# Kernel optimization log

Measured on AMD Instinct MI355X. Metric: run time of the kernel, lower is better.

Reference implementation:

```python
import jax, jax.numpy as jnp
import numpy as np

EPS = 1e-5

def setup_inputs() -> dict:
    key = jax.random.key(0)
    ks = jax.random.split(key, 4)
    n, c, h, w = 4, 256, 64, 64
    attn_chans = 64
    x = jax.random.normal(ks[0], (n, c, h, w), dtype=jnp.float32)
    gamma = jnp.ones((c,), jnp.float32)
    beta = jnp.zeros((c,), jnp.float32)
    qkv_w = jax.random.normal(ks[1], (c, 3 * c), dtype=jnp.float32) / np.sqrt(c)
    proj_w = jax.random.normal(ks[2], (c, c), dtype=jnp.float32) / np.sqrt(c)
    proj_b = jnp.zeros((c,), jnp.float32)
    return {"x": x, "gamma": gamma, "beta": beta, "qkv_w": qkv_w,
            "proj_w": proj_w, "proj_b": proj_b, "attn_chans": attn_chans}


def reference(x, gamma, beta, qkv_w, proj_w, proj_b, attn_chans):
    n, c, h, w = x.shape
    heads = c // attn_chans
    scale = attn_chans ** 0.5
    # BatchNorm2d (training mode: batch statistics, biased variance)
    mean = jnp.mean(x, axis=(0, 2, 3))
    var = jnp.var(x, axis=(0, 2, 3))
    xn = (x - mean[:, None, None]) * jax.lax.rsqrt(var + EPS)[:, None, None]
    xn = xn * gamma[:, None, None] + beta[:, None, None]
    # (n, c, h, w) -> (n, hw, c)
    seq = jnp.transpose(xn.reshape(n, c, h * w), (0, 2, 1))
    qkv = seq @ qkv_w                             # (n, hw, 3c)
    # faithful to torch: view (n, hw, 3c) as (n, heads, hw, 3*attn_chans)
    qkv = qkv.reshape(n, heads, h * w, 3 * attn_chans)
    q, k, v = jnp.split(qkv, 3, axis=-1)          # each (n, heads, hw, d)
    scores = jnp.einsum('nhqd,nhkd->nhqk', q, k) / scale
    attn = jax.nn.softmax(scores, axis=-1)
    o = jnp.einsum('nhqk,nhkd->nhqd', attn, v)    # (n, heads, hw, d)
    o = o.reshape(n, h * w, heads * attn_chans)   # (n, hw, c)
    out = o @ proj_w + proj_b                     # (n, hw, c)
    return jnp.transpose(out, (0, 2, 1)).reshape(n, c, h, w)
```

## Files before the change

### kernel.cpp

```cpp
#include <hip/hip_runtime.h>
#include <stdint.h>

#define NB 4
#define CCH 256
#define HW 4096
#define HEADS 4
#define DH 64
#define SLEN 4096
#define EPSV 1e-5f
#define NEG_INF (-__builtin_inff())
#define QSCALE (0.125f * 1.44269504088896340736f)

typedef unsigned short u16;
typedef __bf16 bf16x8 __attribute__((ext_vector_type(8)));
typedef float f32x4 __attribute__((ext_vector_type(4)));

__device__ __forceinline__ u16 f2bf(float f) {
  union { float f; uint32_t u; } v; v.f = f;
  uint32_t r = v.u + 0x7FFFu + ((v.u >> 16) & 1u);
  return (u16)(r >> 16);
}

__global__ __launch_bounds__(256) void k_bnstats(
    const float* __restrict__ x, const float* __restrict__ gamma,
    const float* __restrict__ beta, float* __restrict__ ab) {
  int ch = blockIdx.x, t = threadIdx.x;
  float s = 0.f, ss = 0.f;
  for (int n = 0; n < NB; ++n) {
    const float4* p = (const float4*)(x + ((size_t)(n * CCH + ch)) * HW);
    for (int i = t; i < HW / 4; i += 256) {
      float4 v = p[i];
      s += v.x + v.y + v.z + v.w;
      ss += v.x * v.x + v.y * v.y + v.z * v.z + v.w * v.w;
    }
  }
#pragma unroll
  for (int m = 32; m >= 1; m >>= 1) {
    s += __shfl_down(s, m);
    ss += __shfl_down(ss, m);
  }
  __shared__ float ls[4], lss[4];
  if ((t & 63) == 0) { ls[t >> 6] = s; lss[t >> 6] = ss; }
  __syncthreads();
  if (t == 0) {
    float S = 0.f, SS = 0.f;
    for (int i = 0; i < 4; ++i) { S += ls[i]; SS += lss[i]; }
    float inv = 1.0f / (float)(NB * HW);
    float mean = S * inv;
    float var = SS * inv - mean * mean;
    float a = gamma[ch] * rsqrtf(var + EPSV);
    ab[ch] = a;
    ab[CCH + ch] = beta[ch] - mean * a;
  }
}

__global__ __launch_bounds__(256) void k_seq(
    const float* __restrict__ x, const float* __restrict__ ab,
    u16* __restrict__ seq) {
  __shared__ float tile[64][65];
  int pb = blockIdx.x * 64, cb = blockIdx.y * 64, n = blockIdx.z;
  int t = threadIdx.x;
  {
    int cl = t >> 2, pc = (t & 3) * 16;
    float a = ab[cb + cl], b = ab[CCH + cb + cl];
    const float* src = x + ((size_t)(n * CCH + cb + cl)) * HW + pb + pc;
#pragma unroll
    for (int i = 0; i < 4; ++i) {
      float4 v = *(const float4*)(src + i * 4);
      tile[cl][pc + i * 4 + 0] = v.x * a + b;
      tile[cl][pc + i * 4 + 1] = v.y * a + b;
      tile[cl][pc + i * 4 + 2] = v.z * a + b;
      tile[cl][pc + i * 4 + 3] = v.w * a + b;
    }
  }
  __syncthreads();
  {
    int pl = t >> 2, cs = (t & 3) * 16;
    union { u16 u[16]; uint4 v[2]; } tmp;
#pragma unroll
    for (int i = 0; i < 16; ++i) tmp.u[i] = f2bf(tile[cs + i][pl]);
    u16* dst = seq + ((size_t)(n * HW + pb + pl)) * CCH + cb + cs;
    *(uint4*)dst = tmp.v[0];
    *(uint4*)(dst + 8) = tmp.v[1];
  }
}

__global__ __launch_bounds__(256) void k_cvt(
    const float* __restrict__ qw, const float* __restrict__ pw,
    u16* __restrict__ qwb, u16* __restrict__ pwb) {
  int i = (blockIdx.x * 256 + threadIdx.x) * 4;
  const int NQ = CCH * 3 * CCH;
  union { u16 u[4]; uint2 v2; } o;
  if (i < NQ) {
    float4 v = *(const float4*)(qw + i);
    o.u[0] = f2bf(v.x); o.u[1] = f2bf(v.y); o.u[2] = f2bf(v.z); o.u[3] = f2bf(v.w);
    *(uint2*)(qwb + i) = o.v2;
  } else {
    int j = i - NQ;
    float4 v = *(const float4*)(pw + j);
    o.u[0] = f2bf(v.x); o.u[1] = f2bf(v.y); o.u[2] = f2bf(v.z); o.u[3] = f2bf(v.w);
    *(uint2*)(pwb + j) = o.v2;
  }
}

__global__ __launch_bounds__(256) void k_qkv(
    const u16* __restrict__ seq, const u16* __restrict__ w,
    u16* __restrict__ Q, u16* __restrict__ K, u16* __restrict__ Vt) {
  __shared__ __attribute__((aligned(16))) u16 As[64 * 32];
  __shared__ __attribute__((aligned(16))) u16 Bs[64 * 32];
  int Rb = blockIdx.x * 64, Cb = blockIdx.y * 64;
  int t = threadIdx.x, lane = t & 63, wv = t >> 6;
  int wr = (wv >> 1) * 32, wc = (wv & 1) * 32;
  f32x4 acc[2][2] = {};
  for (int kb = 0; kb < CCH; kb += 32) {
    {
      int r = t >> 2, kc = t & 3;
      uint4 v = *(const uint4*)(seq + ((size_t)(Rb + r)) * CCH + kb + kc * 8);
      *(uint4*)((char*)As + r * 64 + ((kc * 16) ^ ((r & 3) << 4))) = v;
    }
    {
      int k = t >> 3, jc = (t & 7) * 8;
      union { u16 u[8]; uint4 v; } tmp;
      tmp.v = *(const uint4*)(w + ((size_t)(kb + k)) * 768 + Cb + jc);
#pragma unroll
      for (int i2 = 0; i2 < 8; ++i2) {
        int j = jc + i2;
        *(u16*)((char*)Bs + j * 64 + ((k * 2) ^ ((j & 3) << 4))) = tmp.u[i2];
      }
    }
    __syncthreads();
    bf16x8 af[2], bfr[2];
#pragma unroll
    for (int f = 0; f < 2; ++f) {
      int row = wr + f * 16 + (lane & 15);
      af[f] = *(const bf16x8*)((const char*)As + row * 64 +
                               (((lane >> 4) * 16) ^ ((row & 3) << 4)));
      int col = wc + f * 16 + (lane & 15);
      bfr[f] = *(const bf16x8*)((const char*)Bs + col * 64 +
                                (((lane >> 4) * 16) ^ ((col & 3) << 4)));
    }
#pragma unroll
    for (int i2 = 0; i2 < 2; ++i2)
#pragma unroll
      for (int j2 = 0; j2 < 2; ++j2)
        acc[i2][j2] = __builtin_amdgcn_mfma_f32_16x16x32_bf16(af[i2], bfr[j2], acc[i2][j2], 0, 0, 0);
    __syncthreads();
  }
#pragma unroll
  for (int i2 = 0; i2 < 2; ++i2)
#pragma unroll
    for (int j2 = 0; j2 < 2; ++j2)
#pragma unroll
      for (int e = 0; e < 4; ++e) {
        int R = Rb + wr + i2 * 16 + (lane >> 4) * 4 + e;
        int cg = Cb + wc + j2 * 16 + (lane & 15);
        int p = R & (HW - 1);
        int head = p >> 10, mq = p & 1023;
        int qn = mq * 4 + cg / 192, tt = cg % 192;
        int nhx = (R >> 12) * HEADS + head;
        float a = acc[i2][j2][e];
        if (tt < 64)
          Q[((size_t)nhx * SLEN + qn) * DH + tt] = f2bf(a * QSCALE);
        else if (tt < 128)
          K[((size_t)nhx * SLEN + qn) * DH + tt - 64] = f2bf(a);
        else
          Vt[(size_t)nhx * SLEN * DH + (size_t)(tt - 128) * SLEN + qn] = f2bf(a);
      }
}

__global__ __launch_bounds__(128, 2) void k_attn(
    const u16* __restrict__ Q, const u16* __restrict__ K,
    const u16* __restrict__ Vt, u16* __restrict__ O) {
  __shared__ __attribute__((aligned(16))) char smem[16384 + 1024];
  int q0 = blockIdx.x * 64, nh = blockIdx.y;
  int t = threadIdx.x;
  int lane = t & 63, w = t >> 6;
  int l15 = lane & 15, g = lane >> 4;
  size_t base = (size_t)nh * SLEN * DH;
  char* Ps = smem + w * 8192;
  int swz = (l15 & 7) << 4;

  bf16x8 qv[4][2];
#pragma unroll
  for (int qf = 0; qf < 4; ++qf) {
    const u16* qp = Q + base + (size_t)(q0 + qf * 16 + l15) * DH + g * 8;
    qv[qf][0] = *(const bf16x8*)qp;
    qv[qf][1] = *(const bf16x8*)(qp + 32);
  }

  f32x4 o[4][4] = {};
  float m[4] = {NEG_INF, NEG_INF, NEG_INF, NEG_INF};
  float lsum[4] = {0.f, 0.f, 0.f, 0.f};

  const u16* Kbase = K + base + (size_t)l15 * DH + g * 8;
  const u16* Vbase = Vt + base + (size_t)l15 * SLEN + g * 8;

  const int TILES = SLEN / 64 / 2;
  for (int tt = 0; tt < TILES; ++tt) {
    int kv0 = (w * TILES + tt) * 64;
    bf16x8 kf[4][2];
#pragma unroll
    for (int cf = 0; cf < 4; ++cf) {
      const u16* kp = Kbase + (size_t)(kv0 + cf * 16) * DH;
      kf[cf][0] = *(const bf16x8*)kp;
      kf[cf][1] = *(const bf16x8*)(kp + 32);
    }
    bf16x8 vf[4][2];
#pragma unroll
    for (int df = 0; df < 4; ++df) {
      const u16* vp = Vbase + (size_t)(df * 16) * SLEN + kv0;
      vf[df][0] = *(const bf16x8*)vp;
      vf[df][1] = *(const bf16x8*)(vp + 32);
    }
#pragma unroll
    for (int qf = 0; qf < 4; ++qf) {
      f32x4 st[4];
#pragma unroll
      for (int cf = 0; cf < 4; ++cf) {
        f32x4 a = {};
        a = __builtin_amdgcn_mfma_f32_16x16x32_bf16(kf[cf][0], qv[qf][0], a, 0, 0, 0);
        a = __builtin_amdgcn_mfma_f32_16x16x32_bf16(kf[cf][1], qv[qf][1], a, 0, 0, 0);
        st[cf] = a;
      }
      float mx = st[0][0];
#pragma unroll
      for (int cf = 0; cf < 4; ++cf)
#pragma unroll
        for (int e = 0; e < 4; ++e) mx = fmaxf(mx, st[cf][e]);
      mx = fmaxf(mx, __shfl_xor(mx, 16));
      mx = fmaxf(mx, __shfl_xor(mx, 32));
      float mn = fmaxf(m[qf], mx);
      float al = exp2f(m[qf] - mn);
      m[qf] = mn;
      lsum[qf] *= al;
#pragma unroll
      for (int e = 0; e < 4; ++e) {
        float ae = __shfl(al, (lane & 48) | (((lane >> 4) << 2) + e));
#pragma unroll
        for (int df = 0; df < 4; ++df) o[qf][df][e] *= ae;
      }
      float ls = 0.f;
#pragma unroll
      for (int cf = 0; cf < 4; ++cf) {
        union { __bf16 h[4]; uint2 v; } pk;
#pragma unroll
        for (int e = 0; e < 4; ++e) {
          float p = exp2f(st[cf][e] - mn);
          ls += p;
          pk.h[e] = (__bf16)p;
        }
        *(uint2*)(Ps + (qf * 16 + l15) * 128 + ((cf * 32 + g * 8) ^ swz)) = pk.v;
      }
      lsum[qf] += ls;
    }
#pragma unroll
    for (int qf = 0; qf < 4; ++qf) {
#pragma unroll
      for (int ks = 0; ks < 2; ++ks) {
        bf16x8 pa = *(const bf16x8*)(Ps + (qf * 16 + l15) * 128 + ((ks * 64 + g * 16) ^ swz));
#pragma unroll
        for (int df = 0; df < 4; ++df)
          o[qf][df] = __builtin_amdgcn_mfma_f32_16x16x32_bf16(pa, vf[df][ks], o[qf][df], 0, 0, 0);
      }
    }
  }
#pragma unroll
  for (int qf = 0; qf < 4; ++qf) {
    lsum[qf] += __shfl_xor(lsum[qf], 16);
    lsum[qf] += __shfl_xor(lsum[qf], 32);
  }
  __syncthreads();
  float* Om = (float*)smem;
  float* mlb = (float*)(smem + 16384);
  if (w == 1) {
#pragma unroll
    for (int qf = 0; qf < 4; ++qf)
#pragma unroll
      for (int df = 0; df < 4; ++df) {
        int d = df * 16 + l15;
        int ba = d * 256 + qf * 64 + g * 16;
        *(f32x4*)((char*)smem + (ba ^ ((d & 7) << 4))) = o[qf][df];
      }
  }
  if (lane < 16) {
#pragma unroll
    for (int qf = 0; qf < 4; ++qf) {
      mlb[((w * 4 + qf) * 2 + 0) * 16 + l15] = m[qf];
      mlb[((w * 4 + qf) * 2 + 1) * 16 + l15] = lsum[qf];
    }
  }
  __syncthreads();
  if (w == 0) {
    int n = nh >> 2, head = nh & 3;
#pragma unroll
    for (int qf = 0; qf < 4; ++qf) {
      f32x4 m0 = *(f32x4*)&mlb[((0 + qf) * 2 + 0) * 16 + g * 4];
      f32x4 l0 = *(f32x4*)&mlb[((0 + qf) * 2 + 1) * 16 + g * 4];
      f32x4 m1 = *(f32x4*)&mlb[((4 + qf) * 2 + 0) * 16 + g * 4];
      f32x4 l1 = *(f32x4*)&mlb[((4 + qf) * 2 + 1) * 16 + g * 4];
      float a0[4], a1[4], rinv[4];
#pragma unroll
      for (int e = 0; e < 4; ++e) {
        float mf = fmaxf(m0[e], m1[e]);
        a0[e] = exp2f(m0[e] - mf);
        a1[e] = exp2f(m1[e] - mf);
        rinv[e] = 1.f / (l0[e] * a0[e] + l1[e] * a1[e]);
      }
#pragma unroll
      for (int df = 0; df < 4; ++df) {
        int d = df * 16 + l15;
        int ba = d * 256 + qf * 64 + g * 16;
        f32x4 o1 = *(f32x4*)((char*)smem + (ba ^ ((d & 7) << 4)));
#pragma unroll
        for (int e = 0; e < 4; ++e) {
          int qn = q0 + qf * 16 + g * 4 + e;
          float val = (o[qf][df][e] * a0[e] + o1[e] * a1[e]) * rinv[e];
          size_t off = (((size_t)n * HW) + head * 1024 + (qn >> 2)) * CCH + (qn & 3) * DH + d;
          O[off] = f2bf(val);
        }
      }
    }
  }
}

__global__ __launch_bounds__(256) void k_proj(
    const u16* __restrict__ A, const u16* __restrict__ W,
    const float* __restrict__ bias, float* __restrict__ out) {
  __shared__ __attribute__((aligned(16))) u16 As[64 * 32];
  __shared__ __attribute__((aligned(16))) u16 Bs[64 * 32];
  int Rb = blockIdx.x * 64, Cb = blockIdx.y * 64;
  int t = threadIdx.x, lane = t & 63, wv = t >> 6;
  int wr = (wv >> 1) * 32, wc = (wv & 1) * 32;
  f32x4 acc[2][2] = {};
  for (int kb = 0; kb < CCH; kb += 32) {
    {
      int r = t >> 2, kc = t & 3;
      uint4 v = *(const uint4*)(A + ((size_t)(Rb + r)) * CCH + kb + kc * 8);
      *(uint4*)((char*)As + r * 64 + ((kc * 16) ^ ((r & 3) << 4))) = v;
    }
    {
      int k = t >> 3, jc = (t & 7) * 8;
      union { u16 u[8]; uint4 v; } tmp;
      tmp.v = *(const uint4*)(W + ((size_t)(kb + k)) * CCH + Cb + jc);
#pragma unroll
      for (int i2 = 0; i2 < 8; ++i2) {
        int j = jc + i2;
        *(u16*)((char*)Bs + j * 64 + ((k * 2) ^ ((j & 3) << 4))) = tmp.u[i2];
      }
    }
    __syncthreads();
    bf16x8 af[2], bfr[2];
#pragma unroll
    for (int f = 0; f < 2; ++f) {
      int row = wr + f * 16 + (lane & 15);
      af[f] = *(const bf16x8*)((const char*)As + row * 64 +
                               (((lane >> 4) * 16) ^ ((row & 3) << 4)));
      int col = wc + f * 16 + (lane & 15);
      bfr[f] = *(const bf16x8*)((const char*)Bs + col * 64 +
                                (((lane >> 4) * 16) ^ ((col & 3) << 4)));
    }
#pragma unroll
    for (int i2 = 0; i2 < 2; ++i2)
#pragma unroll
      for (int j2 = 0; j2 < 2; ++j2)
        acc[i2][j2] = __builtin_amdgcn_mfma_f32_16x16x32_bf16(af[i2], bfr[j2], acc[i2][j2], 0, 0, 0);
    __syncthreads();
  }
#pragma unroll
  for (int i2 = 0; i2 < 2; ++i2)
#pragma unroll
    for (int j2 = 0; j2 < 2; ++j2)
#pragma unroll
      for (int e = 0; e < 4; ++e) {
        int R = Rb + wr + i2 * 16 + (lane >> 4) * 4 + e;
        int cg = Cb + wc + j2 * 16 + (lane & 15);
        out[((size_t)((R >> 12) * CCH + cg)) * HW + (R & (HW - 1))] =
            acc[i2][j2][e] + bias[cg];
      }
}

extern "C" void kernel_launch(void* const* d_in, const int* in_sizes, int n_in,
                              void* d_out, int out_size, void* d_ws, size_t ws_size,
                              hipStream_t stream) {
  (void)in_sizes; (void)n_in; (void)out_size; (void)ws_size;
  const float* x      = (const float*)d_in[0];
  const float* gamma  = (const float*)d_in[1];
  const float* beta   = (const float*)d_in[2];
  const float* qkv_w  = (const float*)d_in[3];
  const float* proj_w = (const float*)d_in[4];
  const float* proj_b = (const float*)d_in[5];

  char* ws = (char*)d_ws;
  size_t off = 0;
  float* ab = (float*)(ws + off); off += 4096;
  u16* seq  = (u16*)(ws + off);  off += (size_t)NB * HW * CCH * 2;
  u16* qwb  = (u16*)(ws + off);  off += (size_t)CCH * 3 * CCH * 2;
  u16* pwb  = (u16*)(ws + off);  off += (size_t)CCH * CCH * 2;
  u16* Qb   = (u16*)(ws + off);  off += (size_t)NB * HEADS * SLEN * DH * 2;
  u16* Kb   = (u16*)(ws + off);  off += (size_t)NB * HEADS * SLEN * DH * 2;
  u16* Vtb  = (u16*)(ws + off);  off += (size_t)NB * HEADS * SLEN * DH * 2;
  u16* oseq = (u16*)(ws + off);  off += (size_t)NB * HW * CCH * 2;

  k_bnstats<<<256, 256, 0, stream>>>(x, gamma, beta, ab);
  k_seq<<<dim3(HW / 64, CCH / 64, NB), 256, 0, stream>>>(x, ab, seq);
  k_cvt<<<256, 256, 0, stream>>>(qkv_w, proj_w, qwb, pwb);
  k_qkv<<<dim3((NB * HW) / 64, 768 / 64), 256, 0, stream>>>(seq, qwb, Qb, Kb, Vtb);
  k_attn<<<dim3(SLEN / 64, NB * HEADS), 128, 0, stream>>>(Qb, Kb, Vtb, oseq);
  k_proj<<<dim3((NB * HW) / 64, CCH / 64), 256, 0, stream>>>(oseq, pwb, proj_b, (float*)d_out);
}
```

Baseline: 298.4 us.

## Split attention KV across four waves, add lazy rescale, fuse prep kernels

The attention kernel now uses four waves per block, each handling a quarter of the key/value sequence, and combines their partial softmax states in a two-level tree through shared memory. The online-softmax rescale is skipped unless the running max grows by more than 8 (log2 units), which removes exp and multiply work on most tiles. The BN-statistics and weight-conversion kernels are fused into one launch, with the conversion now handling 8 elements per thread. The cost is more shared memory and extra barrier stages in the merge, and exp2 values can reach up to 2^8 before renormalisation, which could affect bf16 accuracy.

```diff
diff --git a/kernel.cpp b/kernel.cpp
--- a/kernel.cpp
+++ b/kernel.cpp
@@ -21,36 +21,52 @@
   return (u16)(r >> 16);
 }
 
-__global__ __launch_bounds__(256) void k_bnstats(
+__global__ __launch_bounds__(256) void k_pre(
     const float* __restrict__ x, const float* __restrict__ gamma,
-    const float* __restrict__ beta, float* __restrict__ ab) {
-  int ch = blockIdx.x, t = threadIdx.x;
-  float s = 0.f, ss = 0.f;
-  for (int n = 0; n < NB; ++n) {
-    const float4* p = (const float4*)(x + ((size_t)(n * CCH + ch)) * HW);
-    for (int i = t; i < HW / 4; i += 256) {
-      float4 v = p[i];
-      s += v.x + v.y + v.z + v.w;
-      ss += v.x * v.x + v.y * v.y + v.z * v.z + v.w * v.w;
-    }
-  }
-#pragma unroll
-  for (int m = 32; m >= 1; m >>= 1) {
-    s += __shfl_down(s, m);
-    ss += __shfl_down(ss, m);
-  }
-  __shared__ float ls[4], lss[4];
-  if ((t & 63) == 0) { ls[t >> 6] = s; lss[t >> 6] = ss; }
-  __syncthreads();
-  if (t == 0) {
-    float S = 0.f, SS = 0.f;
-    for (int i = 0; i < 4; ++i) { S += ls[i]; SS += lss[i]; }
-    float inv = 1.0f / (float)(NB * HW);
-    float mean = S * inv;
-    float var = SS * inv - mean * mean;
-    float a = gamma[ch] * rsqrtf(var + EPSV);
-    ab[ch] = a;
-    ab[CCH + ch] = beta[ch] - mean * a;
+    const float* __restrict__ beta, const float* __restrict__ qw,
+    const float* __restrict__ pw, float* __restrict__ ab,
+    u16* __restrict__ qwb, u16* __restrict__ pwb) {
+  int t = threadIdx.x;
+  if (blockIdx.x < 256) {
+    int ch = blockIdx.x;
+    float s = 0.f, ss = 0.f;
+    for (int n = 0; n < NB; ++n) {
+      const float4* p = (const float4*)(x + ((size_t)(n * CCH + ch)) * HW);
+      for (int i = t; i < HW / 4; i += 256) {
+        float4 v = p[i];
+        s += v.x + v.y + v.z + v.w;
+        ss += v.x * v.x + v.y * v.y + v.z * v.z + v.w * v.w;
+      }
+    }
+#pragma unroll
+    for (int mm = 32; mm >= 1; mm >>= 1) {
+      s += __shfl_down(s, mm);
+      ss += __shfl_down(ss, mm);
+    }
+    __shared__ float ls[4], lss[4];
+    if ((t & 63) == 0) { ls[t >> 6] = s; lss[t >> 6] = ss; }
+    __syncthreads();
+    if (t == 0) {
+      float S = 0.f, SS = 0.f;
+      for (int i = 0; i < 4; ++i) { S += ls[i]; SS += lss[i]; }
+      float inv = 1.0f / (float)(NB * HW);
+      float mean = S * inv;
+      float var = SS * inv - mean * mean;
+      float a = gamma[ch] * rsqrtf(var + EPSV);
+      ab[ch] = a;
+      ab[CCH + ch] = beta[ch] - mean * a;
+    }
+  } else {
+    const int NQ = CCH * 3 * CCH;
+    int i = ((blockIdx.x - 256) * 256 + t) * 8;
+    const float* src = (i < NQ) ? (qw + i) : (pw + (i - NQ));
+    u16* dst = (i < NQ) ? (qwb + i) : (pwb + (i - NQ));
+    float4 v0 = *(const float4*)src;
+    float4 v1 = *(const float4*)(src + 4);
+    union { u16 u[8]; uint4 v; } o;
+    o.u[0] = f2bf(v0.x); o.u[1] = f2bf(v0.y); o.u[2] = f2bf(v0.z); o.u[3] = f2bf(v0.w);
+    o.u[4] = f2bf(v1.x); o.u[5] = f2bf(v1.y); o.u[6] = f2bf(v1.z); o.u[7] = f2bf(v1.w);
+    *(uint4*)dst = o.v;
   }
 }
 
@@ -82,24 +98,6 @@
     u16* dst = seq + ((size_t)(n * HW + pb + pl)) * CCH + cb + cs;
     *(uint4*)dst = tmp.v[0];
     *(uint4*)(dst + 8) = tmp.v[1];
-  }
-}
-
-__global__ __launch_bounds__(256) void k_cvt(
-    const float* __restrict__ qw, const float* __restrict__ pw,
-    u16* __restrict__ qwb, u16* __restrict__ pwb) {
-  int i = (blockIdx.x * 256 + threadIdx.x) * 4;
-  const int NQ = CCH * 3 * CCH;
-  union { u16 u[4]; uint2 v2; } o;
-  if (i < NQ) {
-    float4 v = *(const float4*)(qw + i);
-    o.u[0] = f2bf(v.x); o.u[1] = f2bf(v.y); o.u[2] = f2bf(v.z); o.u[3] = f2bf(v.w);
-    *(uint2*)(qwb + i) = o.v2;
-  } else {
-    int j = i - NQ;
-    float4 v = *(const float4*)(pw + j);
-    o.u[0] = f2bf(v.x); o.u[1] = f2bf(v.y); o.u[2] = f2bf(v.z); o.u[3] = f2bf(v.w);
-    *(uint2*)(pwb + j) = o.v2;
   }
 }
 
@@ -168,13 +166,14 @@
       }
 }
 
-__global__ __launch_bounds__(128, 2) void k_attn(
+__global__ __launch_bounds__(256, 2) void k_attn(
     const u16* __restrict__ Q, const u16* __restrict__ K,
     const u16* __restrict__ Vt, u16* __restrict__ O) {
-  __shared__ __attribute__((aligned(16))) char smem[16384 + 1024];
+  __shared__ __attribute__((aligned(16))) char smem[32768 + 2048];
+  float* mlA = (float*)(smem + 32768);
+  float* mlB = (float*)(smem + 32768 + 1024);
   int q0 = blockIdx.x * 64, nh = blockIdx.y;
-  int t = threadIdx.x;
-  int lane = t & 63, w = t >> 6;
+  int t = threadIdx.x, lane = t & 63, w = t >> 6;
   int l15 = lane & 15, g = lane >> 4;
   size_t base = (size_t)nh * SLEN * DH;
   char* Ps = smem + w * 8192;
@@ -195,17 +194,16 @@
   const u16* Kbase = K + base + (size_t)l15 * DH + g * 8;
   const u16* Vbase = Vt + base + (size_t)l15 * SLEN + g * 8;
 
-  const int TILES = SLEN / 64 / 2;
+  const int TILES = SLEN / 64 / 4;
   for (int tt = 0; tt < TILES; ++tt) {
     int kv0 = (w * TILES + tt) * 64;
-    bf16x8 kf[4][2];
+    bf16x8 kf[4][2], vf[4][2];
 #pragma unroll
     for (int cf = 0; cf < 4; ++cf) {
       const u16* kp = Kbase + (size_t)(kv0 + cf * 16) * DH;
       kf[cf][0] = *(const bf16x8*)kp;
       kf[cf][1] = *(const bf16x8*)(kp + 32);
     }
-    bf16x8 vf[4][2];
 #pragma unroll
     for (int df = 0; df < 4; ++df) {
       const u16* vp = Vbase + (size_t)(df * 16) * SLEN + kv0;
@@ -229,15 +227,17 @@
         for (int e = 0; e < 4; ++e) mx = fmaxf(mx, st[cf][e]);
       mx = fmaxf(mx, __shfl_xor(mx, 16));
       mx = fmaxf(mx, __shfl_xor(mx, 32));
-      float mn = fmaxf(m[qf], mx);
-      float al = exp2f(m[qf] - mn);
-      m[qf] = mn;
-      lsum[qf] *= al;
-#pragma unroll
-      for (int e = 0; e < 4; ++e) {
-        float ae = __shfl(al, (lane & 48) | (((lane >> 4) << 2) + e));
-#pragma unroll
-        for (int df = 0; df < 4; ++df) o[qf][df][e] *= ae;
+      if (!__all(mx <= m[qf] + 8.0f)) {
+        float mn = fmaxf(m[qf], mx);
+        float al = exp2f(m[qf] - mn);
+        m[qf] = mn;
+        lsum[qf] *= al;
+#pragma unroll
+        for (int e = 0; e < 4; ++e) {
+          float ae = __shfl(al, (lane & 48) | (((lane >> 4) << 2) + e));
+#pragma unroll
+          for (int df = 0; df < 4; ++df) o[qf][df][e] *= ae;
+        }
       }
       float ls = 0.f;
 #pragma unroll
@@ -245,7 +245,7 @@
         union { __bf16 h[4]; uint2 v; } pk;
 #pragma unroll
         for (int e = 0; e < 4; ++e) {
-          float p = exp2f(st[cf][e] - mn);
+          float p = exp2f(st[cf][e] - m[qf]);
           ls += p;
           pk.h[e] = (__bf16)p;
         }
@@ -269,54 +269,79 @@
     lsum[qf] += __shfl_xor(lsum[qf], 16);
     lsum[qf] += __shfl_xor(lsum[qf], 32);
   }
-  __syncthreads();
-  float* Om = (float*)smem;
-  float* mlb = (float*)(smem + 16384);
-  if (w == 1) {
-#pragma unroll
-    for (int qf = 0; qf < 4; ++qf)
+  f32x4 me[4], le[4];
+#pragma unroll
+  for (int qf = 0; qf < 4; ++qf)
+#pragma unroll
+    for (int e = 0; e < 4; ++e) {
+      int idx = (lane & 48) | (((lane >> 4) & 3) << 2) | e;
+      me[qf][e] = __shfl(m[qf], idx);
+      le[qf][e] = __shfl(lsum[qf], idx);
+    }
+
+  auto publish = [&](char* reg, int s) {
+#pragma unroll
+    for (int qf = 0; qf < 4; ++qf) {
 #pragma unroll
       for (int df = 0; df < 4; ++df) {
         int d = df * 16 + l15;
-        int ba = d * 256 + qf * 64 + g * 16;
-        *(f32x4*)((char*)smem + (ba ^ ((d & 7) << 4))) = o[qf][df];
-      }
-  }
-  if (lane < 16) {
+        *(f32x4*)(reg + ((d * 256 + qf * 64 + g * 16) ^ ((d & 7) << 4))) = o[qf][df];
+      }
+      if (l15 == 0) {
+        *(f32x4*)&mlA[(s * 4 + qf) * 16 + g * 4] = me[qf];
+        *(f32x4*)&mlB[(s * 4 + qf) * 16 + g * 4] = le[qf];
+      }
+    }
+  };
+  auto merge = [&](char* reg, int s) {
 #pragma unroll
     for (int qf = 0; qf < 4; ++qf) {
-      mlb[((w * 4 + qf) * 2 + 0) * 16 + l15] = m[qf];
-      mlb[((w * 4 + qf) * 2 + 1) * 16 + l15] = lsum[qf];
-    }
-  }
+      f32x4 mp = *(f32x4*)&mlA[(s * 4 + qf) * 16 + g * 4];
+      f32x4 lp = *(f32x4*)&mlB[(s * 4 + qf) * 16 + g * 4];
+      f32x4 op[4];
+#pragma unroll
+      for (int df = 0; df < 4; ++df) {
+        int d = df * 16 + l15;
+        op[df] = *(f32x4*)(reg + ((d * 256 + qf * 64 + g * 16) ^ ((d & 7) << 4)));
+      }
+#pragma unroll
+      for (int e = 0; e < 4; ++e) {
+        float mf = fmaxf(me[qf][e], mp[e]);
+        float as = exp2f(me[qf][e] - mf), ap = exp2f(mp[e] - mf);
+        le[qf][e] = le[qf][e] * as + lp[e] * ap;
+        me[qf][e] = mf;
+#pragma unroll
+        for (int df = 0; df < 4; ++df)
+          o[qf][df][e] = o[qf][df][e] * as + op[df][e] * ap;
+      }
+    }
+  };
+
+  __syncthreads();
+  if (w == 1) publish(smem, 1);
+  if (w == 3) publish(smem + 16384, 3);
+  __syncthreads();
+  if (w == 0) merge(smem, 1);
+  if (w == 2) merge(smem + 16384, 3);
+  __syncthreads();
+  if (w == 2) publish(smem, 2);
   __syncthreads();
   if (w == 0) {
+    merge(smem, 2);
     int n = nh >> 2, head = nh & 3;
 #pragma unroll
     for (int qf = 0; qf < 4; ++qf) {
-      f32x4 m0 = *(f32x4*)&mlb[((0 + qf) * 2 + 0) * 16 + g * 4];
-      f32x4 l0 = *(f32x4*)&mlb[((0 + qf) * 2 + 1) * 16 + g * 4];
-      f32x4 m1 = *(f32x4*)&mlb[((4 + qf) * 2 + 0) * 16 + g * 4];
-      f32x4 l1 = *(f32x4*)&mlb[((4 + qf) * 2 + 1) * 16 + g * 4];
-      float a0[4], a1[4], rinv[4];
-#pragma unroll
-      for (int e = 0; e < 4; ++e) {
-        float mf = fmaxf(m0[e], m1[e]);
-        a0[e] = exp2f(m0[e] - mf);
-        a1[e] = exp2f(m1[e] - mf);
-        rinv[e] = 1.f / (l0[e] * a0[e] + l1[e] * a1[e]);
-      }
+      f32x4 rinv;
+#pragma unroll
+      for (int e = 0; e < 4; ++e) rinv[e] = 1.f / le[qf][e];
 #pragma unroll
       for (int df = 0; df < 4; ++df) {
         int d = df * 16 + l15;
-        int ba = d * 256 + qf * 64 + g * 16;
-        f32x4 o1 = *(f32x4*)((char*)smem + (ba ^ ((d & 7) << 4)));
 #pragma unroll
         for (int e = 0; e < 4; ++e) {
           int qn = q0 + qf * 16 + g * 4 + e;
-          float val = (o[qf][df][e] * a0[e] + o1[e] * a1[e]) * rinv[e];
           size_t off = (((size_t)n * HW) + head * 1024 + (qn >> 2)) * CCH + (qn & 3) * DH + d;
-          O[off] = f2bf(val);
+          O[off] = f2bf(o[qf][df][e] * rinv[e]);
         }
       }
     }
@@ -401,10 +426,9 @@
   u16* Vtb  = (u16*)(ws + off);  off += (size_t)NB * HEADS * SLEN * DH * 2;
   u16* oseq = (u16*)(ws + off);  off += (size_t)NB * HW * CCH * 2;
 
-  k_bnstats<<<256, 256, 0, stream>>>(x, gamma, beta, ab);
+  k_pre<<<384, 256, 0, stream>>>(x, gamma, beta, qkv_w, proj_w, ab, qwb, pwb);
   k_seq<<<dim3(HW / 64, CCH / 64, NB), 256, 0, stream>>>(x, ab, seq);
-  k_cvt<<<256, 256, 0, stream>>>(qkv_w, proj_w, qwb, pwb);
   k_qkv<<<dim3((NB * HW) / 64, 768 / 64), 256, 0, stream>>>(seq, qwb, Qb, Kb, Vtb);
-  k_attn<<<dim3(SLEN / 64, NB * HEADS), 128, 0, stream>>>(Qb, Kb, Vtb, oseq);
+  k_attn<<<dim3(SLEN / 64, NB * HEADS), 256, 0, stream>>>(Qb, Kb, Vtb, oseq);
   k_proj<<<dim3((NB * HW) / 64, CCH / 64), 256, 0, stream>>>(oseq, pwb, proj_b, (float*)d_out);
 }
```

Result: faster. 277.2 us (-7.1%).
